# Kernel optimization log

Hardware: AMD Instinct MI355X
Metric: run time of the kernel (lower is better)

The kernel has to match this reference:

```python
import jax, jax.numpy as jnp
import numpy as np

BANDWIDTH = 1.0
DRIFT_COEF = 1.0
NEG_DRIFT_COEF = 0.5
EPS = 1e-8

B, TA, DA = 4096, 16, 8


def setup_inputs() -> dict:
    key = jax.random.key(0)
    k1, k2, k3 = jax.random.split(key, 3)
    x = jax.random.normal(k1, (B, TA, DA), dtype=jnp.float32)
    y_pos = jax.random.normal(k2, (B, TA, DA), dtype=jnp.float32)
    y_neg = jax.random.normal(k3, (B, TA, DA), dtype=jnp.float32)
    return {"x": x, "y_pos": y_pos, "y_neg": y_neg}


def _drift_field(x_flat, y_flat, sign):
    """Nadaraya-Watson weighted average of pairwise diffs, fused via norms+matmul.

    Equivalent to: sign * sum_j wn_ij * (x_i - y_j)
    where wn = row-normalized RBF kernel with masked diagonal.
    """
    b = x_flat.shape[0]
    x_sq = jnp.sum(x_flat * x_flat, axis=1)
    y_sq = jnp.sum(y_flat * y_flat, axis=1)
    d2 = x_sq[:, None] + y_sq[None, :] - 2.0 * (x_flat @ y_flat.T)
    d2 = jnp.maximum(d2, 0.0)
    w = jnp.exp(-d2 / (2.0 * BANDWIDTH ** 2))
    # mask self-interaction (mask_self=True)
    w = w * (1.0 - jnp.eye(b, dtype=w.dtype))
    s = jnp.sum(w, axis=1, keepdims=True)               # (B, 1)
    denom = jnp.maximum(s, EPS)
    wn = w / denom                                       # (B, B)
    # sum_j wn_ij (x_i - y_j) = x_i * rowsum(wn)_i - wn @ y
    diff_avg = x_flat * (s / denom) - wn @ y_flat        # (B, D)
    return sign * diff_avg


def reference(x, y_pos, y_neg):
    b = x.shape[0]
    x_flat = x.reshape(b, -1)
    yp_flat = y_pos.reshape(b, -1)
    yn_flat = y_neg.reshape(b, -1)
    # V_pos = wn_pos @ (-(x_i - y_j)); V_neg = wn_neg @ (x_i - y_j)
    v = DRIFT_COEF * _drift_field(x_flat, yp_flat, -1.0)
    v = v + NEG_DRIFT_COEF * _drift_field(x_flat, yn_flat, 1.0)
    return v.reshape(x.shape)
```

## Files before the change

kernel.cpp:

```cpp
#include <hip/hip_runtime.h>
#include <math.h>


#define EPSV 1e-8f
#define CUTOFF 160.0f
#define LCAP 512
#define RCAP 64

typedef unsigned int uint;
typedef unsigned short ushort;
typedef __attribute__((ext_vector_type(8))) short bf16x8;
typedef __attribute__((ext_vector_type(4))) float f32x4;

#define CNT_IDX 20480u
#define COUNTS_IDX 20481u
#define REGION_BYTE 131072u
#define OVF_BYTE 1310720u
#define OVF_CAP 98304u
#define XA_BYTE 2097152u
#define MAT_BYTES 3145728u
#define WS_NEED 11534336u

static __device__ __forceinline__ ushort bf16_rne(float v) {
    uint u = __float_as_uint(v);
    uint r = (u + 0x7FFFu + ((u >> 16) & 1u)) >> 16;
    return (ushort)r;
}
static __device__ __forceinline__ float bf16_f(ushort h) {
    return __uint_as_float(((uint)h) << 16);
}

typedef const __attribute__((address_space(1))) uint guint;
typedef __attribute__((address_space(3))) uint luint;
static __device__ __forceinline__ void lds_load16(const void* g, void* l) {
    __builtin_amdgcn_global_load_lds((guint*)g, (luint*)l, 16, 0, 0);
}

__global__ __launch_bounds__(256) void prep_k(
    const float* __restrict__ x, const float* __restrict__ yp,
    const float* __restrict__ yn, float* __restrict__ ws,
    unsigned char* __restrict__ wsb)
{
    __shared__ ushort hi_s[4][128];
    __shared__ ushort lo_s[4][128];
    const int t = threadIdx.x, wv = t >> 6, lane = t & 63;
    const int rid = blockIdx.x * 4 + wv;
    const int seg = rid >> 12;
    const int row = rid & 4095;
    const float* src = (seg == 0) ? x : (seg == 1) ? yp : yn;

    float2 v = ((const float2*)(src + (size_t)row * 128))[lane];
    float ss = v.x * v.x + v.y * v.y;
    #pragma unroll
    for (int off = 32; off > 0; off >>= 1) ss += __shfl_down(ss, off);
    if (lane == 0) ws[8192 + seg * 4096 + row] = ss;

    ushort h0 = bf16_rne(v.x), h1 = bf16_rne(v.y);
    ushort l0 = bf16_rne(v.x - bf16_f(h0));
    ushort l1 = bf16_rne(v.y - bf16_f(h1));
    hi_s[wv][2 * lane] = h0; hi_s[wv][2 * lane + 1] = h1;
    lo_s[wv][2 * lane] = l0; lo_s[wv][2 * lane + 1] = l1;
    __syncthreads();

    uint* dst = (uint*)(wsb + XA_BYTE + (size_t)seg * MAT_BYTES) + (size_t)row * 192;
    #pragma unroll
    for (int q = 0; q < 3; ++q) {
        const int w = q * 64 + lane;
        const int K = 2 * w;
        const int g = K >> 6, c = (K >> 3) & 7, off = K & 7;
        const int Klog = (g << 6) + ((c ^ (row & 7)) << 3) + off;
        const int hseg = Klog >> 7, kk = Klog & 127;
        const int islo = (seg == 0) ? (hseg == 1) : (hseg == 2);
        const ushort* arr = islo ? lo_s[wv] : hi_s[wv];
        dst[w] = (uint)arr[kk] | ((uint)arr[kk + 1] << 16);
    }

    const int gid = blockIdx.x * 256 + t;
    if (gid < 8192) ws[gid] = 0.0f;
    if (gid >= 8192 && gid < 8192 + 2049)
        ((uint*)ws)[CNT_IDX + (gid - 8192)] = 0u;
}

__global__ __launch_bounds__(256) void phase_a_mfma(
    const unsigned char* __restrict__ wsb, float* __restrict__ wsf, unsigned ovfcap)
{
    const int f = blockIdx.z;
    const ushort* __restrict__ XA = (const ushort*)(wsb + XA_BYTE);
    const ushort* __restrict__ YB = (const ushort*)(wsb + XA_BYTE + (f ? 2u : 1u) * MAT_BYTES);
    const float* __restrict__ xsq = wsf + 8192;
    const float* __restrict__ ysq = wsf + (f ? 16384 : 12288);
    uint* cnt     = (uint*)wsf + CNT_IDX;
    uint* counts  = (uint*)wsf + COUNTS_IDX;
    uint2* region = (uint2*)(wsb + REGION_BYTE);
    uint2* ovf    = (uint2*)(wsb + OVF_BYTE);

    __shared__ ushort As[128 * 64];
    __shared__ ushort Bs[128 * 64];
    __shared__ uint2 pbuf[LCAP];
    __shared__ uint pcnt, obase;

    const int t = threadIdx.x;
    const int lane = t & 63, wv = t >> 6;
    const int wr = wv >> 1, wc = wv & 1;
    const int i0 = blockIdx.y * 128, j0 = blockIdx.x * 128;
    const int m = lane & 15, qd = lane >> 4;
    const uint b = (uint)blockIdx.z * 1024u + (uint)blockIdx.y * 32u + (uint)blockIdx.x;

    if (t == 0) pcnt = 0;

    f32x4 acc[4][4];
    #pragma unroll
    for (int a = 0; a < 4; ++a)
        #pragma unroll
        for (int bb = 0; bb < 4; ++bb) acc[a][bb] = (f32x4)0.0f;

    const int srow = lane >> 3;
    const int scol = lane & 7;

    for (int k0 = 0; k0 < 384; k0 += 64) {
        #pragma unroll
        for (int q = 0; q < 4; ++q) {
            const int grp = 4 * wv + q;
            const int r = grp * 8 + srow;
            const ushort* ga = XA + (size_t)(i0 + r) * 384 + k0 + scol * 8;
            const ushort* gb = YB + (size_t)(j0 + r) * 384 + k0 + scol * 8;
            lds_load16(ga, &As[grp * 512]);
            lds_load16(gb, &Bs[grp * 512]);
        }
        __syncthreads();
        #pragma unroll
        for (int ks = 0; ks < 2; ++ks) {
            bf16x8 av[4], bv[4];
            #pragma unroll
            for (int ff = 0; ff < 4; ++ff) {
                const int ra = 64 * wr + 16 * ff + m;
                const int ca = (4 * ks + qd) ^ (m & 7);
                av[ff] = *(const bf16x8*)&As[ra * 64 + ca * 8];
                const int rb = 64 * wc + 16 * ff + m;
                const int cb = (4 * ks + qd) ^ (m & 7);
                bv[ff] = *(const bf16x8*)&Bs[rb * 64 + cb * 8];
            }
            #pragma unroll
            for (int fi = 0; fi < 4; ++fi)
                #pragma unroll
                for (int fj = 0; fj < 4; ++fj)
                    acc[fi][fj] = __builtin_amdgcn_mfma_f32_16x16x32_bf16(
                        av[fi], bv[fj], acc[fi][fj], 0, 0, 0);
        }
        __syncthreads();
    }

    float xq[4][4], yq[4];
    #pragma unroll
    for (int fi = 0; fi < 4; ++fi)
        #pragma unroll
        for (int rg = 0; rg < 4; ++rg)
            xq[fi][rg] = xsq[i0 + 64 * wr + 16 * fi + 4 * qd + rg];
    #pragma unroll
    for (int fj = 0; fj < 4; ++fj)
        yq[fj] = ysq[j0 + 64 * wc + 16 * fj + m];

    #pragma unroll
    for (int fi = 0; fi < 4; ++fi) {
        #pragma unroll
        for (int fj = 0; fj < 4; ++fj) {
            #pragma unroll
            for (int rg = 0; rg < 4; ++rg) {
                const int i = i0 + 64 * wr + 16 * fi + 4 * qd + rg;
                const int j = j0 + 64 * wc + 16 * fj + m;
                float d2 = xq[fi][rg] + yq[fj] - 2.0f * acc[fi][fj][rg];
                if (d2 < CUTOFF && i != j) {
                    float w = __expf(-0.5f * fmaxf(d2, 0.0f));
                    uint li = atomicAdd(&pcnt, 1u);
                    if (li < LCAP)
                        pbuf[li] = make_uint2(
                            (uint)i | ((uint)j << 12) | ((uint)f << 24),
                            __float_as_uint(w));
                }
            }
        }
    }
    __syncthreads();
    uint n = pcnt; if (n > LCAP) n = LCAP;
    const uint nr = (n > RCAP) ? RCAP : n;
    if (t == 0) {
        counts[b] = nr;
        if (n > RCAP) obase = atomicAdd(cnt, n - RCAP);
    }
    __syncthreads();
    for (uint p = t; p < n; p += 256) {
        uint2 pr = pbuf[p];
        if (p < RCAP) {
            region[b * RCAP + p] = pr;
        } else {
            uint gi = obase + (p - RCAP);
            if (gi < ovfcap) ovf[gi] = pr;
        }
        atomicAdd(&wsf[((pr.x >> 24) & 1u) * 4096u + (pr.x & 0xFFFu)],
                  __uint_as_float(pr.y));
    }
}

__global__ __launch_bounds__(256) void phase_a_f32(
    const float* __restrict__ x, const float* __restrict__ yp,
    const float* __restrict__ yn, float* __restrict__ ws,
    unsigned char* __restrict__ wsb, unsigned ovfcap)
{
    const int f = blockIdx.z;
    const float* __restrict__ Y   = f ? yn : yp;
    const float* __restrict__ xsq = ws + 8192;
    const float* __restrict__ ysq = ws + (f ? 16384 : 12288);
    float* __restrict__ S         = ws + (f ? 4096 : 0);
    unsigned* cnt = (unsigned*)ws + CNT_IDX;
    uint2* ovf    = (uint2*)(wsb + OVF_BYTE);

    __shared__ float xs[32][128 + 4];
    __shared__ float ys[32][128 + 4];

    const int t  = threadIdx.x;
    const int tx = t & 15, ty = t >> 4;
    const int i0 = blockIdx.y * 128, j0 = blockIdx.x * 128;

    float acc[8][8];
    #pragma unroll
    for (int a = 0; a < 8; ++a)
        #pragma unroll
        for (int bb = 0; bb < 8; ++bb) acc[a][bb] = 0.f;

    const int ldr = t >> 1;
    const int ldk = (t & 1) * 16;

    for (int k0 = 0; k0 < 128; k0 += 32) {
        #pragma unroll
        for (int q = 0; q < 4; ++q) {
            float4 vx = *(const float4*)&x[(size_t)(i0 + ldr) * 128 + k0 + ldk + 4 * q];
            float4 vy = *(const float4*)&Y[(size_t)(j0 + ldr) * 128 + k0 + ldk + 4 * q];
            const int kb = ldk + 4 * q;
            xs[kb + 0][ldr] = vx.x; xs[kb + 1][ldr] = vx.y;
            xs[kb + 2][ldr] = vx.z; xs[kb + 3][ldr] = vx.w;
            ys[kb + 0][ldr] = vy.x; ys[kb + 1][ldr] = vy.y;
            ys[kb + 2][ldr] = vy.z; ys[kb + 3][ldr] = vy.w;
        }
        __syncthreads();
        #pragma unroll 4
        for (int kk = 0; kk < 32; ++kk) {
            float4 a0 = *(const float4*)&xs[kk][8 * ty];
            float4 a1 = *(const float4*)&xs[kk][8 * ty + 4];
            float4 b0 = *(const float4*)&ys[kk][8 * tx];
            float4 b1 = *(const float4*)&ys[kk][8 * tx + 4];
            float av[8] = {a0.x, a0.y, a0.z, a0.w, a1.x, a1.y, a1.z, a1.w};
            float bv[8] = {b0.x, b0.y, b0.z, b0.w, b1.x, b1.y, b1.z, b1.w};
            #pragma unroll
            for (int di = 0; di < 8; ++di)
                #pragma unroll
                for (int dj = 0; dj < 8; ++dj)
                    acc[di][dj] = fmaf(av[di], bv[dj], acc[di][dj]);
        }
        __syncthreads();
    }

    float xqv[8], yqv[8], srow[8];
    #pragma unroll
    for (int di = 0; di < 8; ++di) { xqv[di] = xsq[i0 + 8 * ty + di]; srow[di] = 0.f; }
    #pragma unroll
    for (int dj = 0; dj < 8; ++dj) yqv[dj] = ysq[j0 + 8 * tx + dj];

    #pragma unroll
    for (int di = 0; di < 8; ++di) {
        const int i = i0 + 8 * ty + di;
        #pragma unroll
        for (int dj = 0; dj < 8; ++dj) {
            const int j = j0 + 8 * tx + dj;
            float d2 = fmaxf(xqv[di] + yqv[dj] - 2.0f * acc[di][dj], 0.0f);
            if (i != j) {
                float w = __expf(-0.5f * d2);
                srow[di] += w;
                if (d2 < CUTOFF) {
                    unsigned idx = atomicAdd(cnt, 1u);
                    if (idx < ovfcap)
                        ovf[idx] = make_uint2(
                            (unsigned)i | ((unsigned)j << 12) | ((unsigned)f << 24),
                            __float_as_uint(w));
                }
            }
        }
    }
    #pragma unroll
    for (int di = 0; di < 8; ++di) {
        float v = srow[di];
        #pragma unroll
        for (int off = 8; off > 0; off >>= 1) v += __shfl_down(v, off, 16);
        if (tx == 0) atomicAdd(&S[i0 + 8 * ty + di], v);
    }
}

__global__ __launch_bounds__(256) void finalize_k(
    const float* __restrict__ x, const float* __restrict__ ws,
    float* __restrict__ out)
{
    const int gid = blockIdx.x * 256 + threadIdx.x;
    const int i = gid >> 7;
    float spv = ws[i], snv = ws[4096 + i];
    float c = 0.5f * snv / fmaxf(snv, EPSV) - spv / fmaxf(spv, EPSV);
    out[gid] = x[gid] * c;
}

__global__ __launch_bounds__(256) void scatter_k(
    const float* __restrict__ yp, const float* __restrict__ yn,
    const float* __restrict__ ws, const unsigned char* __restrict__ wsb,
    float* __restrict__ out, unsigned ovfcap)
{
    const uint* counts  = (const uint*)ws + COUNTS_IDX;
    const uint2* region = (const uint2*)(wsb + REGION_BYTE);
    const uint2* ovf    = (const uint2*)(wsb + OVF_BYTE);
    const uint b = blockIdx.x;
    const uint t = threadIdx.x;
    const uint k = t & 127u, ph = t >> 7;

    const uint n = counts[b];
    for (uint p = ph; p < n; p += 2) {
        const uint2 pr = region[b * RCAP + p];
        const uint i  = pr.x & 0xFFFu;
        const uint j  = (pr.x >> 12) & 0xFFFu;
        const uint fb = (pr.x >> 24) & 1u;
        const float w = __uint_as_float(pr.y);
        const float den  = fmaxf(ws[fb * 4096u + i], EPSV);
        const float coef = fb ? (-0.5f / den) : (1.0f / den);
        const float* Yv  = fb ? yn : yp;
        atomicAdd(&out[i * 128u + k], coef * w * Yv[j * 128u + k]);
    }

    uint m = *((const uint*)ws + CNT_IDX); if (m > ovfcap) m = ovfcap;
    const uint total = m * 128u;
    for (uint u = b * 256u + t; u < total; u += 2048u * 256u) {
        const uint p = u >> 7, kk = u & 127u;
        const uint2 pr = ovf[p];
        const uint i  = pr.x & 0xFFFu;
        const uint j  = (pr.x >> 12) & 0xFFFu;
        const uint fb = (pr.x >> 24) & 1u;
        const float w = __uint_as_float(pr.y);
        const float den  = fmaxf(ws[fb * 4096u + i], EPSV);
        const float coef = fb ? (-0.5f / den) : (1.0f / den);
        const float* Yv  = fb ? yn : yp;
        atomicAdd(&out[i * 128u + kk], coef * w * Yv[j * 128u + kk]);
    }
}

extern "C" void kernel_launch(void* const* d_in, const int* in_sizes, int n_in,
                              void* d_out, int out_size, void* d_ws, size_t ws_size,
                              hipStream_t stream)
{
    const float* x  = (const float*)d_in[0];
    const float* yp = (const float*)d_in[1];
    const float* yn = (const float*)d_in[2];
    float* out = (float*)d_out;
    float* ws  = (float*)d_ws;
    unsigned char* wsb = (unsigned char*)d_ws;

    unsigned ovfcap = OVF_CAP;
    if (ws_size < 2097152u)
        ovfcap = (ws_size > OVF_BYTE + 8) ? (unsigned)((ws_size - OVF_BYTE) / 8) : 0u;
    const bool use_mfma = (ws_size >= WS_NEED);

    dim3 ga(32, 32, 2);
    prep_k<<<3072, 256, 0, stream>>>(x, yp, yn, ws, wsb);
    if (use_mfma) {
        phase_a_mfma<<<ga, 256, 0, stream>>>(wsb, ws, ovfcap);
    } else {
        phase_a_f32<<<ga, 256, 0, stream>>>(x, yp, yn, ws, wsb, ovfcap);
    }
    finalize_k<<<2048, 256, 0, stream>>>(x, ws, out);
    scatter_k<<<2048, 256, 0, stream>>>(yp, yn, ws, wsb, out, ovfcap);
}
```

Before: 120.8 us.

## Screen pairs with single bf16 MFMA and recompute survivors' weights in fp32

Replaces the 3-term split-bf16 (hi/lo) product with a single bf16 MFMA pass, used only to screen candidate pairs against a slightly widened cutoff. For each surviving pair, a wavefront recomputes the exact fp32 dot product from the original inputs, then computes the weight and accumulates the row sum. This cuts the MFMA K-loop and workspace traffic by three times. In exchange it adds per-candidate global gathers, and it risks missing pairs near the cutoff if the bf16 error exceeds the margin.

```diff
diff --git a/kernel.cpp b/kernel.cpp
--- a/kernel.cpp
+++ b/kernel.cpp
@@ -3,7 +3,7 @@
 
 
 #define EPSV 1e-8f
-#define CUTOFF 160.0f
+#define CUTOFF_F 162.0f
 #define LCAP 512
 #define RCAP 64
 
@@ -18,17 +18,14 @@
 #define OVF_BYTE 1310720u
 #define OVF_CAP 98304u
 #define XA_BYTE 2097152u
-#define MAT_BYTES 3145728u
-#define WS_NEED 11534336u
+#define MAT_BYTES 1048576u
+#define WS_NEED 5242880u
 
 static __device__ __forceinline__ ushort bf16_rne(float v) {
     uint u = __float_as_uint(v);
     uint r = (u + 0x7FFFu + ((u >> 16) & 1u)) >> 16;
     return (ushort)r;
 }
-static __device__ __forceinline__ float bf16_f(ushort h) {
-    return __uint_as_float(((uint)h) << 16);
-}
 
 typedef const __attribute__((address_space(1))) uint guint;
 typedef __attribute__((address_space(3))) uint luint;
@@ -39,10 +36,9 @@
 __global__ __launch_bounds__(256) void prep_k(
     const float* __restrict__ x, const float* __restrict__ yp,
     const float* __restrict__ yn, float* __restrict__ ws,
-    unsigned char* __restrict__ wsb)
+    unsigned char* __restrict__ wsb, int build)
 {
     __shared__ ushort hi_s[4][128];
-    __shared__ ushort lo_s[4][128];
     const int t = threadIdx.x, wv = t >> 6, lane = t & 63;
     const int rid = blockIdx.x * 4 + wv;
     const int seg = rid >> 12;
@@ -55,24 +51,15 @@
     for (int off = 32; off > 0; off >>= 1) ss += __shfl_down(ss, off);
     if (lane == 0) ws[8192 + seg * 4096 + row] = ss;
 
-    ushort h0 = bf16_rne(v.x), h1 = bf16_rne(v.y);
-    ushort l0 = bf16_rne(v.x - bf16_f(h0));
-    ushort l1 = bf16_rne(v.y - bf16_f(h1));
-    hi_s[wv][2 * lane] = h0; hi_s[wv][2 * lane + 1] = h1;
-    lo_s[wv][2 * lane] = l0; lo_s[wv][2 * lane + 1] = l1;
-    __syncthreads();
-
-    uint* dst = (uint*)(wsb + XA_BYTE + (size_t)seg * MAT_BYTES) + (size_t)row * 192;
-    #pragma unroll
-    for (int q = 0; q < 3; ++q) {
-        const int w = q * 64 + lane;
-        const int K = 2 * w;
+    if (build) {
+        hi_s[wv][2 * lane]     = bf16_rne(v.x);
+        hi_s[wv][2 * lane + 1] = bf16_rne(v.y);
+        __syncthreads();
+        const int K = 2 * lane;
         const int g = K >> 6, c = (K >> 3) & 7, off = K & 7;
         const int Klog = (g << 6) + ((c ^ (row & 7)) << 3) + off;
-        const int hseg = Klog >> 7, kk = Klog & 127;
-        const int islo = (seg == 0) ? (hseg == 1) : (hseg == 2);
-        const ushort* arr = islo ? lo_s[wv] : hi_s[wv];
-        dst[w] = (uint)arr[kk] | ((uint)arr[kk + 1] << 16);
+        uint* dst = (uint*)(wsb + XA_BYTE + (size_t)seg * MAT_BYTES) + (size_t)row * 64;
+        dst[lane] = (uint)hi_s[wv][Klog] | ((uint)hi_s[wv][Klog + 1] << 16);
     }
 
     const int gid = blockIdx.x * 256 + t;
@@ -82,21 +69,26 @@
 }
 
 __global__ __launch_bounds__(256) void phase_a_mfma(
-    const unsigned char* __restrict__ wsb, float* __restrict__ wsf, unsigned ovfcap)
+    const float* __restrict__ x, const float* __restrict__ yp,
+    const float* __restrict__ yn,
+    const unsigned char* __restrict__ wsb, float* __restrict__ wsf,
+    unsigned ovfcap)
 {
     const int f = blockIdx.z;
     const ushort* __restrict__ XA = (const ushort*)(wsb + XA_BYTE);
     const ushort* __restrict__ YB = (const ushort*)(wsb + XA_BYTE + (f ? 2u : 1u) * MAT_BYTES);
+    const float* __restrict__ Yg  = f ? yn : yp;
     const float* __restrict__ xsq = wsf + 8192;
     const float* __restrict__ ysq = wsf + (f ? 16384 : 12288);
+    float* __restrict__ S         = wsf + (f ? 4096 : 0);
     uint* cnt     = (uint*)wsf + CNT_IDX;
     uint* counts  = (uint*)wsf + COUNTS_IDX;
-    uint2* region = (uint2*)(wsb + REGION_BYTE);
-    uint2* ovf    = (uint2*)(wsb + OVF_BYTE);
+    uint2* region = (uint2*)((unsigned char*)wsf + REGION_BYTE);
+    uint2* ovf    = (uint2*)((unsigned char*)wsf + OVF_BYTE);
 
     __shared__ ushort As[128 * 64];
     __shared__ ushort Bs[128 * 64];
-    __shared__ uint2 pbuf[LCAP];
+    __shared__ uint pbuf[LCAP];
     __shared__ uint pcnt, obase;
 
     const int t = threadIdx.x;
@@ -117,13 +109,13 @@
     const int srow = lane >> 3;
     const int scol = lane & 7;
 
-    for (int k0 = 0; k0 < 384; k0 += 64) {
+    for (int k0 = 0; k0 < 128; k0 += 64) {
         #pragma unroll
         for (int q = 0; q < 4; ++q) {
             const int grp = 4 * wv + q;
             const int r = grp * 8 + srow;
-            const ushort* ga = XA + (size_t)(i0 + r) * 384 + k0 + scol * 8;
-            const ushort* gb = YB + (size_t)(j0 + r) * 384 + k0 + scol * 8;
+            const ushort* ga = XA + (size_t)(i0 + r) * 128 + k0 + scol * 8;
+            const ushort* gb = YB + (size_t)(j0 + r) * 128 + k0 + scol * 8;
             lds_load16(ga, &As[grp * 512]);
             lds_load16(gb, &Bs[grp * 512]);
         }
@@ -168,14 +160,11 @@
             for (int rg = 0; rg < 4; ++rg) {
                 const int i = i0 + 64 * wr + 16 * fi + 4 * qd + rg;
                 const int j = j0 + 64 * wc + 16 * fj + m;
-                float d2 = xq[fi][rg] + yq[fj] - 2.0f * acc[fi][fj][rg];
-                if (d2 < CUTOFF && i != j) {
-                    float w = __expf(-0.5f * fmaxf(d2, 0.0f));
+                float d2a = xq[fi][rg] + yq[fj] - 2.0f * acc[fi][fj][rg];
+                if (d2a < CUTOFF_F && i != j) {
                     uint li = atomicAdd(&pcnt, 1u);
                     if (li < LCAP)
-                        pbuf[li] = make_uint2(
-                            (uint)i | ((uint)j << 12) | ((uint)f << 24),
-                            __float_as_uint(w));
+                        pbuf[li] = (uint)i | ((uint)j << 12) | ((uint)f << 24);
                 }
             }
         }
@@ -188,16 +177,26 @@
         if (n > RCAP) obase = atomicAdd(cnt, n - RCAP);
     }
     __syncthreads();
-    for (uint p = t; p < n; p += 256) {
-        uint2 pr = pbuf[p];
-        if (p < RCAP) {
-            region[b * RCAP + p] = pr;
-        } else {
-            uint gi = obase + (p - RCAP);
-            if (gi < ovfcap) ovf[gi] = pr;
-        }
-        atomicAdd(&wsf[((pr.x >> 24) & 1u) * 4096u + (pr.x & 0xFFFu)],
-                  __uint_as_float(pr.y));
+    for (uint p = wv; p < n; p += 4) {
+        const uint pk = pbuf[p];
+        const uint i = pk & 0xFFFu, j = (pk >> 12) & 0xFFFu;
+        float2 xa = ((const float2*)(x + (size_t)i * 128))[lane];
+        float2 yb = ((const float2*)(Yg + (size_t)j * 128))[lane];
+        float d = xa.x * yb.x + xa.y * yb.y;
+        #pragma unroll
+        for (int off = 32; off > 0; off >>= 1) d += __shfl_down(d, off);
+        if (lane == 0) {
+            float d2 = fmaxf(xsq[i] + ysq[j] - 2.0f * d, 0.0f);
+            float w = __expf(-0.5f * d2);
+            atomicAdd(&S[i], w);
+            uint2 pr = make_uint2(pk, __float_as_uint(w));
+            if (p < RCAP) {
+                region[b * RCAP + p] = pr;
+            } else {
+                uint gi = obase + (p - RCAP);
+                if (gi < ovfcap) ovf[gi] = pr;
+            }
+        }
     }
 }
 
@@ -275,7 +274,7 @@
             if (i != j) {
                 float w = __expf(-0.5f * d2);
                 srow[di] += w;
-                if (d2 < CUTOFF) {
+                if (d2 < CUTOFF_F) {
                     unsigned idx = atomicAdd(cnt, 1u);
                     if (idx < ovfcap)
                         ovf[idx] = make_uint2(
@@ -363,9 +362,9 @@
     const bool use_mfma = (ws_size >= WS_NEED);
 
     dim3 ga(32, 32, 2);
-    prep_k<<<3072, 256, 0, stream>>>(x, yp, yn, ws, wsb);
+    prep_k<<<3072, 256, 0, stream>>>(x, yp, yn, ws, wsb, use_mfma ? 1 : 0);
     if (use_mfma) {
-        phase_a_mfma<<<ga, 256, 0, stream>>>(wsb, ws, ovfcap);
+        phase_a_mfma<<<ga, 256, 0, stream>>>(x, yp, yn, wsb, ws, ovfcap);
     } else {
         phase_a_f32<<<ga, 256, 0, stream>>>(x, yp, yn, ws, wsb, ovfcap);
     }
```

New measurement: 104.7 us. 1.15x faster.
